# Optimization experiments

Hardware: AMD Instinct MI355X
Metric: run time of the kernel (lower is better)

## Reference

```python
import jax, jax.numpy as jnp
import numpy as np

N, T, C = 4, 2048, 1024
H = 16
D = C // H  # head_dim = 64


def setup_inputs() -> dict:
    key = jax.random.key(0)
    ks = jax.random.split(key, 6)
    s = 1.0 / np.sqrt(C)
    return {
        "x": jax.random.normal(ks[0], (N, T, C), dtype=jnp.float32),
        "Wq": jax.random.normal(ks[1], (C, C), dtype=jnp.float32) * s,
        "Wk": jax.random.normal(ks[2], (C, C), dtype=jnp.float32) * s,
        "Wv": jax.random.normal(ks[3], (C, C), dtype=jnp.float32) * s,
        "Wo": jax.random.normal(ks[4], (C, C), dtype=jnp.float32) * s,
        "bo": jax.random.normal(ks[5], (C,), dtype=jnp.float32) * s,
    }


def reference(x, Wq, Wk, Wv, Wo, bo):
    n, t, c = x.shape
    # torch nn.Linear: y = x @ W.T
    q = (x @ Wq.T).reshape(n, t, H, D).transpose(0, 2, 1, 3)  # [N,H,T,D]
    k = (x @ Wk.T).reshape(n, t, H, D).transpose(0, 2, 1, 3)
    v = (x @ Wv.T).reshape(n, t, H, D).transpose(0, 2, 1, 3)
    # NOTE: module scales by sqrt(embed_dim), not sqrt(head_dim)
    energy = jnp.einsum("nhqd,nhkd->nhqk", q, k) / jnp.sqrt(jnp.float32(c))
    causal = jnp.tril(jnp.ones((t, t), dtype=bool))  # [T,T]
    energy = jnp.where(causal[None, None], energy, -jnp.inf)
    attn = jax.nn.softmax(energy, axis=-1)
    out = jnp.einsum("nhqk,nhkd->nhqd", attn, v)  # [N,H,T,D]
    out = out.transpose(0, 2, 1, 3).reshape(n, t, c)
    return out @ Wo.T + bo
```

## Files before the change

kernel.cpp:

```cpp
#include <hip/hip_runtime.h>
#include <math.h>

#define N_ 4
#define T_ 2048
#define C_ 1024
#define H_ 16
#define D_ 64
#define NTC (N_*T_*C_)
#define WELEM (C_*C_)

typedef float f32x4  __attribute__((ext_vector_type(4)));
typedef float f32x16 __attribute__((ext_vector_type(16)));
typedef short bf16x8 __attribute__((ext_vector_type(8)));

static __device__ __forceinline__ unsigned short f2bf(float f) {
    union { float f; unsigned u; } v; v.f = f;
    unsigned r = v.u + 0x7FFFu + ((v.u >> 16) & 1u);
    return (unsigned short)(r >> 16);
}

static __device__ __forceinline__ unsigned cvtpk(float lo, float hi) {
    unsigned r;
    asm("v_cvt_pk_bf16_f32 %0, %1, %2" : "=v"(r) : "v"(lo), "v"(hi));
    return r;
}
#define PLSWAP(a, b) asm("v_permlane32_swap_b32 %0, %1" : "+v"(a), "+v"(b))

#define GLDS16(gptr, lptr) \
    __builtin_amdgcn_global_load_lds((const __attribute__((address_space(1))) void*)(gptr), \
                                     (__attribute__((address_space(3))) void*)(lptr), 16, 0, 0)

__global__ __launch_bounds__(256) void cast_x(const float* __restrict__ src,
                                              unsigned short* __restrict__ dst) {
    const int i = blockIdx.x * 256 + threadIdx.x;
    const float4 a = ((const float4*)src)[i * 2];
    const float4 b = ((const float4*)src)[i * 2 + 1];
    unsigned short u[8] = {f2bf(a.x), f2bf(a.y), f2bf(a.z), f2bf(a.w),
                           f2bf(b.x), f2bf(b.y), f2bf(b.z), f2bf(b.w)};
    *(uint4*)&dst[(size_t)i * 8] = *(const uint4*)u;
}

__global__ __launch_bounds__(256) void cast_w4(const float* __restrict__ w0,
                                               const float* __restrict__ w1,
                                               const float* __restrict__ w2,
                                               const float* __restrict__ w3,
                                               unsigned short* __restrict__ dst) {
    const int z = blockIdx.y;
    const float* __restrict__ src = (z == 0) ? w0 : (z == 1) ? w1 : (z == 2) ? w2 : w3;
    unsigned short* __restrict__ d = dst + (size_t)z * WELEM;
    const int i = blockIdx.x * 256 + threadIdx.x;
    const float4 a = ((const float4*)src)[i * 2];
    const float4 b = ((const float4*)src)[i * 2 + 1];
    unsigned short u[8] = {f2bf(a.x), f2bf(a.y), f2bf(a.z), f2bf(a.w),
                           f2bf(b.x), f2bf(b.y), f2bf(b.z), f2bf(b.w)};
    *(uint4*)&d[(size_t)i * 8] = *(const uint4*)u;
}

#define GEMM_BODY(Aptr, Bptr)                                                           \
    __shared__ __align__(16) unsigned short Abuf[128 * 32];                             \
    __shared__ __align__(16) unsigned short Bbuf[128 * 32];                             \
    const int tid  = threadIdx.x;                                                       \
    const int lane = tid & 63;                                                          \
    const int w    = tid >> 6;                                                          \
    const int lo   = lane & 15;                                                         \
    const int hi   = lane >> 4;                                                         \
    const int wm   = w >> 1;                                                            \
    const int wn   = w & 1;                                                             \
    const int rowBase = blockIdx.x * 128;                                               \
    const int colBase = blockIdx.y * 128;                                               \
    f32x4 acc[4][4];                                                                    \
    _Pragma("unroll")                                                                   \
    for (int i = 0; i < 4; ++i)                                                         \
        _Pragma("unroll")                                                               \
        for (int j = 0; j < 4; ++j) acc[i][j] = (f32x4)(0.f);                           \
    const int i0 = tid, i1 = tid + 256;                                                 \
    const int r0 = i0 >> 2, s0_ = i0 & 3, g0 = s0_ ^ ((r0 >> 1) & 3);                   \
    const int r1 = i1 >> 2, s1_ = i1 & 3, g1 = s1_ ^ ((r1 >> 1) & 3);                   \
    const unsigned short* gA0 = (Aptr) + (size_t)(rowBase + r0) * C_ + g0 * 8;          \
    const unsigned short* gA1 = (Aptr) + (size_t)(rowBase + r1) * C_ + g1 * 8;          \
    const unsigned short* gB0 = (Bptr) + (size_t)(colBase + r0) * C_ + g0 * 8;          \
    const unsigned short* gB1 = (Bptr) + (size_t)(colBase + r1) * C_ + g1 * 8;          \
    for (int k0 = 0; k0 < C_; k0 += 32) {                                               \
        GLDS16(gA0 + k0, &Abuf[i0 * 8]);                                                \
        GLDS16(gA1 + k0, &Abuf[i1 * 8]);                                                \
        GLDS16(gB0 + k0, &Bbuf[i0 * 8]);                                                \
        GLDS16(gB1 + k0, &Bbuf[i1 * 8]);                                                \
        __syncthreads();                                                                \
        bf16x8 af[4], bfv[4];                                                           \
        _Pragma("unroll")                                                               \
        for (int mi = 0; mi < 4; ++mi) {                                                \
            const int row = wm * 64 + mi * 16 + lo;                                     \
            const int slot = hi ^ ((row >> 1) & 3);                                     \
            af[mi] = *(const bf16x8*)&Abuf[row * 32 + slot * 8];                        \
        }                                                                               \
        _Pragma("unroll")                                                               \
        for (int ni = 0; ni < 4; ++ni) {                                                \
            const int row = wn * 64 + ni * 16 + lo;                                     \
            const int slot = hi ^ ((row >> 1) & 3);                                     \
            bfv[ni] = *(const bf16x8*)&Bbuf[row * 32 + slot * 8];                       \
        }                                                                               \
        _Pragma("unroll")                                                               \
        for (int mi = 0; mi < 4; ++mi)                                                  \
            _Pragma("unroll")                                                           \
            for (int ni = 0; ni < 4; ++ni)                                              \
                acc[mi][ni] = __builtin_amdgcn_mfma_f32_16x16x32_bf16(af[mi], bfv[ni],  \
                                                                     acc[mi][ni], 0, 0, 0); \
        __syncthreads();                                                                \
    }

__global__ __launch_bounds__(256) void qkv_fused(const unsigned short* __restrict__ A,
                                                 const unsigned short* __restrict__ Wall,
                                                 unsigned short* __restrict__ qkvout) {
    const int z = blockIdx.z;
    const unsigned short* __restrict__ B = Wall + (size_t)z * WELEM;
    unsigned short* __restrict__ Y = qkvout + (size_t)z * NTC;
    const float oscale = (z == 0) ? (0.03125f * 1.44269504f) : 1.0f;

    GEMM_BODY(A, B)

    if (z < 2) {
        #pragma unroll
        for (int mi = 0; mi < 4; ++mi) {
            #pragma unroll
            for (int r = 0; r < 4; ++r) {
                const int row = rowBase + wm * 64 + mi * 16 + hi * 4 + r;
                const int nn = row >> 11, tt = row & (T_ - 1);
                #pragma unroll
                for (int ni = 0; ni < 4; ++ni) {
                    const int col = colBase + wn * 64 + ni * 16 + lo;
                    Y[((size_t)((nn * H_ + (col >> 6)) * T_ + tt)) * D_ + (col & 63)] =
                        f2bf(acc[mi][ni][r] * oscale);
                }
            }
        }
    } else {
        #pragma unroll
        for (int mi = 0; mi < 4; ++mi) {
            #pragma unroll
            for (int r = 0; r < 4; ++r) {
                const int row = rowBase + wm * 64 + mi * 16 + hi * 4 + r;
                const int nn = row >> 11, tt = row & (T_ - 1);
                #pragma unroll
                for (int ni = 0; ni < 4; ++ni) {
                    const int col = colBase + wn * 64 + ni * 16 + lo;
                    Y[(size_t)((nn * 16 + (col >> 6)) * 64 + (col & 63)) * T_ + tt] =
                        f2bf(acc[mi][ni][r]);
                }
            }
        }
    }
}

__global__ __launch_bounds__(256) void out_gemm(const unsigned short* __restrict__ A,
                                                const unsigned short* __restrict__ B,
                                                const float* __restrict__ bo,
                                                float* __restrict__ out) {
    GEMM_BODY(A, B)

    float bias[4];
    #pragma unroll
    for (int ni = 0; ni < 4; ++ni) bias[ni] = bo[colBase + wn * 64 + ni * 16 + lo];
    #pragma unroll
    for (int mi = 0; mi < 4; ++mi) {
        #pragma unroll
        for (int r = 0; r < 4; ++r) {
            const int row = rowBase + wm * 64 + mi * 16 + hi * 4 + r;
            #pragma unroll
            for (int ni = 0; ni < 4; ++ni) {
                const int col = colBase + wn * 64 + ni * 16 + lo;
                out[(size_t)row * C_ + col] = acc[mi][ni][r] + bias[ni];
            }
        }
    }
}

__global__ __launch_bounds__(256, 2) void attn_mfma(const unsigned short* __restrict__ qg,
                                                    const unsigned short* __restrict__ kg,
                                                    const unsigned short* __restrict__ vtg,
                                                    unsigned short* __restrict__ ob) {
    __shared__ __align__(16) unsigned short Kt[2][64 * 64];
    __shared__ __align__(16) unsigned short Vt[2][64 * 64];

    const int tid  = threadIdx.x;
    const int w    = tid >> 6;
    const int lane = tid & 63;
    const int ql   = lane & 31;
    const int h    = lane >> 5;
    const int p    = blockIdx.x >> 6;
    const int nh   = blockIdx.x & 63;
    const size_t base  = (size_t)nh * (T_ * D_);
    const size_t vbase = (size_t)nh * 64 * T_;
    const int nn = nh >> 4, hh = nh & 15;

    const int qt_a = 15 - p, qt_b = p;
    const int nkt_a = 2 * qt_a + 2;
    const int nkt_b = 2 * qt_b + 2;
    const int total = nkt_a + nkt_b;

    const int i0 = tid, i1 = tid + 256;
    const int kr0 = i0 >> 3, kc0 = ((i0 & 7) ^ (kr0 & 7)) * 8;
    const int kr1 = i1 >> 3, kc1 = ((i1 & 7) ^ (kr1 & 7)) * 8;

    #define STAGE(kt_, buf_)                                                            \
        do {                                                                            \
            const int kb_ = (kt_) * 64;                                                 \
            GLDS16(kg + base + (size_t)(kb_ + kr0) * D_ + kc0, &Kt[buf_][i0 * 8]);      \
            GLDS16(kg + base + (size_t)(kb_ + kr1) * D_ + kc1, &Kt[buf_][i1 * 8]);      \
            GLDS16(vtg + vbase + (size_t)kr0 * T_ + kb_ + kc0, &Vt[buf_][i0 * 8]);      \
            GLDS16(vtg + vbase + (size_t)kr1 * T_ + kb_ + kc1, &Vt[buf_][i1 * 8]);      \
        } while (0)

    int qrow0 = qt_a * 128 + w * 32;
    int mynkt = 2 * qt_a + (w >> 1) + 1;
    const int csubdiag = (w & 1) + 1;

    bf16x8 qf[4];
    #pragma unroll
    for (int dsl = 0; dsl < 4; ++dsl)
        qf[dsl] = *(const bf16x8*)(qg + base + (size_t)(qrow0 + ql) * D_ + dsl * 16 + h * 8);

    f32x16 acc0 = (f32x16)(0.f), acc1 = (f32x16)(0.f);
    float mrun = -INFINITY, lrun = 0.f;

    #define EPILOGUE(qr_)                                                               \
        do {                                                                            \
            const float linv = 1.f / lrun;                                              \
            _Pragma("unroll")                                                           \
            for (int r = 0; r < 16; ++r) {                                              \
                const int rc = (r & 3) + 8 * (r >> 2) + 4 * h;                          \
                const float li = __shfl(linv, rc);                                      \
                const size_t rb = (size_t)(nn * T_ + (qr_) + rc) * C_ + hh * 64;        \
                ob[rb + ql]      = f2bf(acc0[r] * li);                                  \
                ob[rb + 32 + ql] = f2bf(acc1[r] * li);                                  \
            }                                                                           \
        } while (0)

    STAGE(0, 0);
    __syncthreads();
    int cur = 0;

    for (int i = 0; i < total; ++i) {
        const int kt = (i < nkt_a) ? i : i - nkt_a;
        if (i + 1 < total) {
            const int ktn = (i + 1 < nkt_a) ? i + 1 : i + 1 - nkt_a;
            STAGE(ktn, cur ^ 1);
        }

        if (i == nkt_a) {
            EPILOGUE(qrow0);
            qrow0 = qt_b * 128 + w * 32;
            mynkt = 2 * qt_b + (w >> 1) + 1;
            #pragma unroll
            for (int dsl = 0; dsl < 4; ++dsl)
                qf[dsl] = *(const bf16x8*)(qg + base + (size_t)(qrow0 + ql) * D_ + dsl * 16 + h * 8);
            acc0 = (f32x16)(0.f); acc1 = (f32x16)(0.f);
            mrun = -INFINITY; lrun = 0.f;
        }

        if (kt < mynkt) {
            const bool diag = (kt == mynkt - 1);
            const int csub = diag ? csubdiag : 2;
            const unsigned short* Kb = Kt[cur];
            const unsigned short* Vb = Vt[cur];

            f32x16 s0, s1;
            __builtin_amdgcn_s_setprio(1);
            {
                f32x16 z = (f32x16)(0.f);
                #pragma unroll
                for (int dsl = 0; dsl < 4; ++dsl) {
                    const bf16x8 ka = *(const bf16x8*)&Kb[ql * 64 + ((dsl * 2 + h) ^ (ql & 7)) * 8];
                    z = __builtin_amdgcn_mfma_f32_32x32x16_bf16(ka, qf[dsl], z, 0, 0, 0);
                }
                s0 = z;
            }
            if (csub > 1) {
                f32x16 z = (f32x16)(0.f);
                #pragma unroll
                for (int dsl = 0; dsl < 4; ++dsl) {
                    const bf16x8 ka = *(const bf16x8*)&Kb[(32 + ql) * 64 + ((dsl * 2 + h) ^ (ql & 7)) * 8];
                    z = __builtin_amdgcn_mfma_f32_32x32x16_bf16(ka, qf[dsl], z, 0, 0, 0);
                }
                s1 = z;
            }
            __builtin_amdgcn_s_setprio(0);

            if (diag) {
                #pragma unroll
                for (int r = 0; r < 16; ++r) {
                    const int rc = (r & 3) + 8 * (r >> 2) + 4 * h;
                    if (csub == 1) { if (rc > ql) s0[r] = -1e30f; }
                    else           { if (rc > ql) s1[r] = -1e30f; }
                }
            }

            float tm = fmaxf(s0[0], s0[1]);
            #pragma unroll
            for (int r = 2; r < 16; r += 2) tm = fmaxf(tm, fmaxf(s0[r], s0[r + 1]));
            if (csub > 1) {
                #pragma unroll
                for (int r = 0; r < 16; r += 2) tm = fmaxf(tm, fmaxf(s1[r], s1[r + 1]));
            }
            tm = fmaxf(tm, __shfl_xor(tm, 32));

            if (!__all(tm <= mrun + 8.f)) {
                const float mnew = fmaxf(mrun, tm);
                const float fsc = exp2f(mrun - mnew);
                mrun = mnew;
                lrun *= fsc;
                #pragma unroll
                for (int r = 0; r < 16; ++r) {
                    const float f = __shfl(fsc, (r & 3) + 8 * (r >> 2) + 4 * h);
                    acc0[r] *= f; acc1[r] *= f;
                }
            }

            float psum = 0.f;
            #pragma unroll
            for (int r = 0; r < 16; ++r) { s0[r] = exp2f(s0[r] - mrun); psum += s0[r]; }
            if (csub > 1) {
                #pragma unroll
                for (int r = 0; r < 16; ++r) { s1[r] = exp2f(s1[r] - mrun); psum += s1[r]; }
            }
            psum += __shfl_xor(psum, 32);
            lrun += psum;

            bf16x8 pa[4];
            #pragma unroll
            for (int a = 0; a < 2; ++a) {
                if (a < csub) {
                    #pragma unroll
                    for (int b = 0; b < 2; ++b) {
                        const f32x16& P = a ? s1 : s0;
                        unsigned w0 = cvtpk(P[8 * b + 0], P[8 * b + 1]);
                        unsigned w1 = cvtpk(P[8 * b + 2], P[8 * b + 3]);
                        unsigned w2 = cvtpk(P[8 * b + 4], P[8 * b + 5]);
                        unsigned w3 = cvtpk(P[8 * b + 6], P[8 * b + 7]);
                        PLSWAP(w0, w2);
                        PLSWAP(w1, w3);
                        unsigned wd[4] = {w0, w1, w2, w3};
                        pa[2 * a + b] = *(bf16x8*)wd;
                    }
                }
            }

            __builtin_amdgcn_s_setprio(1);
            #pragma unroll
            for (int ks = 0; ks < 4; ++ks) {
                if (ks < 2 * csub) {
                    const bf16x8 vf0 = *(const bf16x8*)&Vb[ql * 64 + ((ks * 2 + h) ^ (ql & 7)) * 8];
                    const bf16x8 vf1 = *(const bf16x8*)&Vb[(32 + ql) * 64 + ((ks * 2 + h) ^ (ql & 7)) * 8];
                    acc0 = __builtin_amdgcn_mfma_f32_32x32x16_bf16(pa[ks], vf0, acc0, 0, 0, 0);
                    acc1 = __builtin_amdgcn_mfma_f32_32x32x16_bf16(pa[ks], vf1, acc1, 0, 0, 0);
                }
            }
            __builtin_amdgcn_s_setprio(0);
        }
        __syncthreads();
        cur ^= 1;
    }

    EPILOGUE(qrow0);
    #undef STAGE
    #undef EPILOGUE
}

extern "C" void kernel_launch(void* const* d_in, const int* in_sizes, int n_in,
                              void* d_out, int out_size, void* d_ws, size_t ws_size,
                              hipStream_t stream) {
    const float* x  = (const float*)d_in[0];
    const float* Wq = (const float*)d_in[1];
    const float* Wk = (const float*)d_in[2];
    const float* Wv = (const float*)d_in[3];
    const float* Wo = (const float*)d_in[4];
    const float* bo = (const float*)d_in[5];
    float* out = (float*)d_out;

    unsigned short* ws = (unsigned short*)d_ws;
    unsigned short* x_bf   = ws;
    unsigned short* w_bf   = x_bf + (size_t)NTC;
    unsigned short* qkv_bf = w_bf + (size_t)4 * WELEM;
    unsigned short* a_bf   = qkv_bf + (size_t)3 * NTC;

    cast_x<<<NTC / (8 * 256), 256, 0, stream>>>(x, x_bf);
    dim3 gw(WELEM / (8 * 256), 4);
    cast_w4<<<gw, 256, 0, stream>>>(Wq, Wk, Wv, Wo, w_bf);

    dim3 gq(N_ * T_ / 128, C_ / 128, 3);
    qkv_fused<<<gq, 256, 0, stream>>>(x_bf, w_bf, qkv_bf);

    attn_mfma<<<512, 256, 0, stream>>>(qkv_bf, qkv_bf + (size_t)NTC, qkv_bf + (size_t)2 * NTC, a_bf);

    dim3 gg(N_ * T_ / 128, C_ / 128);
    out_gemm<<<gg, 256, 0, stream>>>(a_bf, w_bf + 3 * (size_t)WELEM, bo, out);
}
```

Baseline: 191.5 us.

## Replace paired causal q-tile blocks with one q-tile per block, heavy-first order

The attention kernel no longer pairs a long and a short causal query tile inside one block. It launches one block per 128-row query tile per head, which gives 1024 blocks instead of 512, and orders them so the tiles with the most key blocks dispatch first. This removes the mid-loop epilogue and Q reload, and relies on the hardware scheduler to balance the uneven causal work. The trade-off is more blocks that each stage their own K/V tiles, plus possible tail imbalance.

```diff
diff --git a/kernel.cpp b/kernel.cpp
--- a/kernel.cpp
+++ b/kernel.cpp
@@ -186,16 +186,25 @@
     const int lane = tid & 63;
     const int ql   = lane & 31;
     const int h    = lane >> 5;
-    const int p    = blockIdx.x >> 6;
-    const int nh   = blockIdx.x & 63;
+    const int bid  = blockIdx.x;
+    const int qtile = 15 - (bid >> 6);
+    const int nh   = bid & 63;
+    const int qb   = qtile * 128;
     const size_t base  = (size_t)nh * (T_ * D_);
     const size_t vbase = (size_t)nh * 64 * T_;
-    const int nn = nh >> 4, hh = nh & 15;
-
-    const int qt_a = 15 - p, qt_b = p;
-    const int nkt_a = 2 * qt_a + 2;
-    const int nkt_b = 2 * qt_b + 2;
-    const int total = nkt_a + nkt_b;
+    const int qrow0 = qb + w * 32;
+
+    bf16x8 qf[4];
+    #pragma unroll
+    for (int dsl = 0; dsl < 4; ++dsl)
+        qf[dsl] = *(const bf16x8*)(qg + base + (size_t)(qrow0 + ql) * D_ + dsl * 16 + h * 8);
+
+    f32x16 acc0 = (f32x16)(0.f), acc1 = (f32x16)(0.f);
+    float mrun = -INFINITY, lrun = 0.f;
+
+    const int mynkt  = (qrow0 >> 6) + 1;
+    const int nktmax = (qb >> 6) + 2;
+    const int csubdiag = (w & 1) + 1;
 
     const int i0 = tid, i1 = tid + 256;
     const int kr0 = i0 >> 3, kc0 = ((i0 & 7) ^ (kr0 & 7)) * 8;
@@ -210,52 +219,12 @@
             GLDS16(vtg + vbase + (size_t)kr1 * T_ + kb_ + kc1, &Vt[buf_][i1 * 8]);      \
         } while (0)
 
-    int qrow0 = qt_a * 128 + w * 32;
-    int mynkt = 2 * qt_a + (w >> 1) + 1;
-    const int csubdiag = (w & 1) + 1;
-
-    bf16x8 qf[4];
-    #pragma unroll
-    for (int dsl = 0; dsl < 4; ++dsl)
-        qf[dsl] = *(const bf16x8*)(qg + base + (size_t)(qrow0 + ql) * D_ + dsl * 16 + h * 8);
-
-    f32x16 acc0 = (f32x16)(0.f), acc1 = (f32x16)(0.f);
-    float mrun = -INFINITY, lrun = 0.f;
-
-    #define EPILOGUE(qr_)                                                               \
-        do {                                                                            \
-            const float linv = 1.f / lrun;                                              \
-            _Pragma("unroll")                                                           \
-            for (int r = 0; r < 16; ++r) {                                              \
-                const int rc = (r & 3) + 8 * (r >> 2) + 4 * h;                          \
-                const float li = __shfl(linv, rc);                                      \
-                const size_t rb = (size_t)(nn * T_ + (qr_) + rc) * C_ + hh * 64;        \
-                ob[rb + ql]      = f2bf(acc0[r] * li);                                  \
-                ob[rb + 32 + ql] = f2bf(acc1[r] * li);                                  \
-            }                                                                           \
-        } while (0)
-
     STAGE(0, 0);
     __syncthreads();
     int cur = 0;
 
-    for (int i = 0; i < total; ++i) {
-        const int kt = (i < nkt_a) ? i : i - nkt_a;
-        if (i + 1 < total) {
-            const int ktn = (i + 1 < nkt_a) ? i + 1 : i + 1 - nkt_a;
-            STAGE(ktn, cur ^ 1);
-        }
-
-        if (i == nkt_a) {
-            EPILOGUE(qrow0);
-            qrow0 = qt_b * 128 + w * 32;
-            mynkt = 2 * qt_b + (w >> 1) + 1;
-            #pragma unroll
-            for (int dsl = 0; dsl < 4; ++dsl)
-                qf[dsl] = *(const bf16x8*)(qg + base + (size_t)(qrow0 + ql) * D_ + dsl * 16 + h * 8);
-            acc0 = (f32x16)(0.f); acc1 = (f32x16)(0.f);
-            mrun = -INFINITY; lrun = 0.f;
-        }
+    for (int kt = 0; kt < nktmax; ++kt) {
+        if (kt + 1 < nktmax) STAGE(kt + 1, cur ^ 1);
 
         if (kt < mynkt) {
             const bool diag = (kt == mynkt - 1);
@@ -360,9 +329,17 @@
         cur ^= 1;
     }
 
-    EPILOGUE(qrow0);
+    const float linv = 1.f / lrun;
+    const int nn = nh >> 4, hh = nh & 15;
+    #pragma unroll
+    for (int r = 0; r < 16; ++r) {
+        const int rc = (r & 3) + 8 * (r >> 2) + 4 * h;
+        const float li = __shfl(linv, rc);
+        const size_t rb = (size_t)(nn * T_ + qrow0 + rc) * C_ + hh * 64;
+        ob[rb + ql]      = f2bf(acc0[r] * li);
+        ob[rb + 32 + ql] = f2bf(acc1[r] * li);
+    }
     #undef STAGE
-    #undef EPILOGUE
 }
 
 extern "C" void kernel_launch(void* const* d_in, const int* in_sizes, int n_in,
@@ -389,7 +366,8 @@
     dim3 gq(N_ * T_ / 128, C_ / 128, 3);
     qkv_fused<<<gq, 256, 0, stream>>>(x_bf, w_bf, qkv_bf);
 
-    attn_mfma<<<512, 256, 0, stream>>>(qkv_bf, qkv_bf + (size_t)NTC, qkv_bf + (size_t)2 * NTC, a_bf);
+    attn_mfma<<<(T_ / 128) * (N_ * H_), 256, 0, stream>>>(
+        qkv_bf, qkv_bf + (size_t)NTC, qkv_bf + (size_t)2 * NTC, a_bf);
 
     dim3 gg(N_ * T_ / 128, C_ / 128);
     out_gemm<<<gg, 256, 0, stream>>>(a_bf, w_bf + 3 * (size_t)WELEM, bo, out);
```

Result: faster. 182.7 us (-4.6%).
